# Kernel tuning notes

Hardware: AMD Instinct MI355X
Metric: run time of the kernel (lower is better)

The kernel has to match this reference:

```python
import jax, jax.numpy as jnp
import numpy as np

NEG_INF = -1e10
SLOPE = 0.01  # LeakyReLU default negative slope

def _lrelu(x):
    return jnp.where(x >= 0, x, SLOPE * x)

def setup_inputs() -> dict:
    key = jax.random.key(0)
    ks = jax.random.split(key, 12)
    B, L, D = 64, 512, 512
    s = 1.0 / np.sqrt(D)
    s2 = 1.0 / np.sqrt(2 * D)
    return {
        "r1": jax.random.normal(ks[0], (B, L, D), jnp.float32),
        "r2": jax.random.normal(ks[1], (B, L, D), jnp.float32),
        "mask1": jax.random.randint(ks[2], (B, L, 1), 0, 2, jnp.int32),
        "mask2": jax.random.randint(ks[3], (B, L, 1), 0, 2, jnp.int32),
        # mlp params (shared for r1 and r2, as in the torch module)
        "W1": jax.random.uniform(ks[4], (D, D), jnp.float32, -s, s),
        "b1": jnp.zeros((D,), jnp.float32),
        "W2": jax.random.uniform(ks[5], (D, D), jnp.float32, -s, s),
        "b2": jnp.zeros((D,), jnp.float32),
        # compare params
        "Wc1": jax.random.uniform(ks[6], (2 * D, D), jnp.float32, -s2, s2),
        "bc1": jnp.zeros((D,), jnp.float32),
        "Wc2": jax.random.uniform(ks[7], (D, D), jnp.float32, -s, s),
        "bc2": jnp.zeros((D,), jnp.float32),
    }

def reference(r1, r2, mask1, mask2, W1, b1, W2, b2, Wc1, bc1, Wc2, bc2):
    # dropout is inference-mode identity
    def mlp(x):
        return _lrelu(_lrelu(x @ W1 + b1) @ W2 + b2)

    def compare(x):
        return _lrelu(_lrelu(x @ Wc1 + bc1) @ Wc2 + bc2)

    m1 = mask1.astype(jnp.float32)  # [B,L1,1]
    m2 = mask2.astype(jnp.float32)  # [B,L2,1]
    r1m = mlp(r1) * m1
    r2m = mlp(r2) * m2

    # pairwise mask: >0 iff both tokens valid (magnitude from the D-dim matmul is irrelevant)
    mpos = m1 * jnp.swapaxes(m2, 1, 2)            # [B,L1,L2] in {0,1}
    mask_inf = jnp.where(mpos > 0, 0.0, NEG_INF)  # additive mask

    o = jnp.einsum('bik,bjk->bij', r1m, r2m) + mask_inf  # [B,L1,L2]
    o1 = jax.nn.softmax(o, axis=2) * mpos
    o2 = jax.nn.softmax(o, axis=1) * mpos

    r1_c = jnp.einsum('bij,bjd->bid', o1, r2m)  # [B,L1,D]
    r2_c = jnp.einsum('bij,bid->bjd', o2, r1m)  # [B,L2,D]

    r1_cmp = compare(jnp.concatenate([r1m, r1_c], axis=-1)) * m1
    r2_cmp = compare(jnp.concatenate([r2m, r2_c], axis=-1)) * m2
    return (r1_cmp, r2_cmp)
```

## Files before the change

### kernel.cpp

```cpp
#include <hip/hip_runtime.h>

#define LRELU_SLOPE 0.01f
#define NEG_BIG -1e10f

typedef unsigned short ushort_t;
typedef __bf16 bf16x8 __attribute__((ext_vector_type(8)));
typedef float f32x4 __attribute__((ext_vector_type(4)));

static __device__ __forceinline__ float lrelu_f(float x) {
    return x >= 0.0f ? x : LRELU_SLOPE * x;
}

static __device__ __forceinline__ ushort_t f2bf(float f) {
    unsigned int u = __float_as_uint(f);
    u += 0x7fffu + ((u >> 16) & 1u);
    return (ushort_t)(u >> 16);
}

static __device__ __forceinline__ void gld_lds16(const ushort_t* g, ushort_t* l) {
    __builtin_amdgcn_global_load_lds((const __attribute__((address_space(1))) void*)g,
                                     (__attribute__((address_space(3))) void*)l,
                                     16, 0, 0);
}

template<bool BIAS, bool LRELU, bool RM, bool PM, bool BF16OUT, bool TWOUT>
__global__ __launch_bounds__(512, 4)
void gemm_nt(const ushort_t* __restrict__ A0, const ushort_t* __restrict__ A1,
             int Ksplit, int lda0, int lda1,
             const ushort_t* __restrict__ B, int ldb,
             const float* __restrict__ bias,
             const int* __restrict__ rm1, const int* __restrict__ rm2,
             void* __restrict__ C, int ldc,
             ushort_t* __restrict__ CT, int Mhalf,
             int M, int N, int K,
             long sA, long sB, long sC)
{
    __shared__ ushort_t As[256 * 64];
    __shared__ ushort_t Bs[128 * 64];

    const unsigned nbx = gridDim.x, nby = gridDim.y;
    unsigned lin = blockIdx.x + nbx * (blockIdx.y + nby * blockIdx.z);
    const unsigned nwg = nbx * nby * gridDim.z;
    if ((nwg & 7u) == 0u)
        lin = (lin & 7u) * (nwg >> 3) + (lin >> 3);
    const unsigned bxs = lin % nbx;
    const unsigned t1  = lin / nbx;
    const unsigned bys = t1 % nby;
    const unsigned bzs = t1 / nby;

    const int bz   = (int)bzs;
    const int tid  = threadIdx.x;
    const int w    = tid >> 6;
    const int lane = tid & 63;
    const int wm   = w >> 1;
    const int wn   = w & 1;
    const int row0 = (int)bys * 256;
    const int col0 = (int)bxs * 128;

    const ushort_t* Ab0 = A0 + (long)bz * sA;
    const ushort_t* Ab1 = A1 + (long)bz * sA;
    const ushort_t* Bb  = B  + (long)bz * sB;

    const int srA = w * 32 + (lane >> 3);
    const int srB = w * 16 + (lane >> 3);
    const int so  = (((lane & 7) ^ ((lane >> 3) & 7)) * 8);

    const int lr = lane & 15, q = lane >> 4;
    const int cx0 = ((q ^ (lr & 7)) * 8);
    const int cx1 = (((q + 4) ^ (lr & 7)) * 8);
    const int aRow = (wm * 64 + lr) * 64;
    const int bRow = (wn * 64 + lr) * 64;

    f32x4 acc[4][4] = {};

    auto stage = [&](int T) {
        const int k0g = T << 6;
        const ushort_t* Ap; int kk0, ldaP;
        if (k0g < Ksplit) { Ap = Ab0; kk0 = k0g;          ldaP = lda0; }
        else              { Ap = Ab1; kk0 = k0g - Ksplit; ldaP = lda1; }
        #pragma unroll
        for (int u = 0; u < 4; ++u)
            gld_lds16(Ap + (size_t)(row0 + srA + u * 8) * ldaP + kk0 + so,
                      As + (w * 32 + u * 8) * 64);
        #pragma unroll
        for (int u = 0; u < 2; ++u)
            gld_lds16(Bb + (size_t)(col0 + srB + u * 8) * ldb + k0g + so,
                      Bs + (w * 16 + u * 8) * 64);
    };

    const int NT = K >> 6;

    for (int T = 0; T < NT; ++T) {
        __builtin_amdgcn_s_barrier();
        asm volatile("" ::: "memory");
        stage(T);
        asm volatile("s_waitcnt vmcnt(0)" ::: "memory");
        __builtin_amdgcn_s_barrier();
        asm volatile("" ::: "memory");

        #pragma unroll
        for (int kk = 0; kk < 2; ++kk) {
            const int cx = kk ? cx1 : cx0;
            bf16x8 af[4], bf[4];
            #pragma unroll
            for (int ii = 0; ii < 4; ++ii)
                af[ii] = *reinterpret_cast<const bf16x8*>(&As[aRow + (ii * 16) * 64 + cx]);
            #pragma unroll
            for (int jj = 0; jj < 4; ++jj)
                bf[jj] = *reinterpret_cast<const bf16x8*>(&Bs[bRow + (jj * 16) * 64 + cx]);
            asm volatile("s_waitcnt lgkmcnt(0)" ::: "memory");
            __builtin_amdgcn_sched_barrier(0);
            __builtin_amdgcn_s_setprio(1);
            #pragma unroll
            for (int ii = 0; ii < 4; ++ii)
                #pragma unroll
                for (int jj = 0; jj < 4; ++jj)
                    acc[ii][jj] = __builtin_amdgcn_mfma_f32_16x16x32_bf16(
                        af[ii], bf[jj], acc[ii][jj], 0, 0, 0);
            __builtin_amdgcn_s_setprio(0);
        }
    }

    float biasv[4];
    int mj[4];
    #pragma unroll
    for (int j = 0; j < 4; ++j) {
        const int c = col0 + wn * 64 + j * 16 + lr;
        if (BIAS) biasv[j] = bias[c];
        if (PM)   mj[j] = rm2[(long)bz * N + c];
    }
    float* Cf = (float*)C + (long)bz * sC;
    ushort_t* Ch = (ushort_t*)C + (long)bz * sC;

    #pragma unroll
    for (int i = 0; i < 4; ++i) {
        const int rg0 = row0 + wm * 64 + i * 16 + q * 4;
        int mi4[4];
        if (RM || PM) {
            #pragma unroll
            for (int r = 0; r < 4; ++r) {
                const int row = rg0 + r;
                if (PM)      mi4[r] = rm1[(long)bz * M + row];
                else         mi4[r] = (row < Mhalf) ? rm1[row] : rm2[row - Mhalf];
            }
        }
        #pragma unroll
        for (int j = 0; j < 4; ++j) {
            const int c = col0 + wn * 64 + j * 16 + lr;
            ushort_t tp[4];
            #pragma unroll
            for (int r = 0; r < 4; ++r) {
                const int row = rg0 + r;
                float v = acc[i][j][r];
                if (BIAS) v += biasv[j];
                if (LRELU) v = lrelu_f(v);
                if (RM) v *= (float)mi4[r];
                if (PM) { if (!(mi4[r] && mj[j])) v += NEG_BIG; }
                const size_t a = (size_t)row * ldc + c;
                if (BF16OUT) Ch[a] = f2bf(v); else Cf[a] = v;
                if (TWOUT) tp[r] = f2bf(v);
            }
            if (TWOUT) {
                const size_t ta = ((size_t)(((rg0 >> 9) + 64) & 127)) * 262144
                                + (size_t)c * 512 + (rg0 & 511);
                *reinterpret_cast<uint2*>(CT + ta) = *reinterpret_cast<uint2*>(tp);
            }
        }
    }
}

__global__ __launch_bounds__(256)
void cvt2_f32_bf16(const float* __restrict__ a, const float* __restrict__ b,
                   ushort_t* __restrict__ oa, ushort_t* __restrict__ ob)
{
    const float* in = blockIdx.y ? b : a;
    ushort_t* out = blockIdx.y ? ob : oa;
    const long i = ((long)blockIdx.x * 256 + threadIdx.x) * 4;
    const float4 v = *reinterpret_cast<const float4*>(in + i);
    ushort_t o[4] = { f2bf(v.x), f2bf(v.y), f2bf(v.z), f2bf(v.w) };
    *reinterpret_cast<uint2*>(out + i) = *reinterpret_cast<uint2*>(o);
}

__global__ __launch_bounds__(256)
void transpose_cvt4(const float* __restrict__ W1, const float* __restrict__ W2,
                    const float* __restrict__ Wc1, const float* __restrict__ Wc2,
                    ushort_t* __restrict__ W1t, ushort_t* __restrict__ W2t,
                    ushort_t* __restrict__ Wc1t, ushort_t* __restrict__ Wc2t)
{
    __shared__ float t[32][33];
    const int z = blockIdx.z;
    const float* in = (z == 0) ? W1 : (z == 1) ? W2 : (z == 2) ? Wc1 : Wc2;
    ushort_t* out   = (z == 0) ? W1t : (z == 1) ? W2t : (z == 2) ? Wc1t : Wc2t;
    const int R = (z == 2) ? 1024 : 512;
    const int C = 512;
    const int c0 = blockIdx.x * 32, r0 = blockIdx.y * 32;
    if (r0 >= R) return;
    const int tx = threadIdx.x & 31, ty = threadIdx.x >> 5;
    #pragma unroll
    for (int p = 0; p < 4; ++p)
        t[ty + p * 8][tx] = in[(size_t)(r0 + ty + p * 8) * C + c0 + tx];
    __syncthreads();
    #pragma unroll
    for (int p = 0; p < 4; ++p)
        out[(size_t)(c0 + ty + p * 8) * R + r0 + tx] = f2bf(t[tx][ty + p * 8]);
}

__global__ __launch_bounds__(256)
void row_stats(const float* __restrict__ o, float* __restrict__ rmax,
               float* __restrict__ rsinv, int L)
{
    const int row  = blockIdx.x * 4 + (threadIdx.x >> 6);
    const int lane = threadIdx.x & 63;
    const float* p = o + (long)row * L;
    float m = -3.0e38f;
    for (int j = lane; j < L; j += 64) m = fmaxf(m, p[j]);
    #pragma unroll
    for (int off = 32; off > 0; off >>= 1) m = fmaxf(m, __shfl_xor(m, off));
    float s = 0.0f;
    for (int j = lane; j < L; j += 64) s += __expf(p[j] - m);
    #pragma unroll
    for (int off = 32; off > 0; off >>= 1) s += __shfl_xor(s, off);
    if (lane == 0) { rmax[row] = m; rsinv[row] = 1.0f / s; }
}

__global__ __launch_bounds__(256)
void col_part(const float* __restrict__ o, float* __restrict__ pm,
              float* __restrict__ ps, int L)
{
    const int b  = blockIdx.z;
    const int rc = blockIdx.y;
    const int j  = blockIdx.x * 256 + threadIdx.x;
    const float* p = o + (long)b * L * L + (long)rc * 64 * L + j;
    float m = -3.0e38f, s = 0.0f;
    #pragma unroll 4
    for (int i = 0; i < 64; ++i) {
        const float x = p[(long)i * L];
        const float mn = fmaxf(m, x);
        s = s * __expf(m - mn) + __expf(x - mn);
        m = mn;
    }
    const long idx = ((long)b * 8 + rc) * L + j;
    pm[idx] = m;
    ps[idx] = s;
}

__global__ __launch_bounds__(256)
void col_combine(const float* __restrict__ pm, const float* __restrict__ ps,
                 float* __restrict__ cmax, float* __restrict__ csinv, int L)
{
    const int b = blockIdx.y;
    const int j = blockIdx.x * 256 + threadIdx.x;
    float mk[8], sk[8];
    #pragma unroll
    for (int k = 0; k < 8; ++k) {
        mk[k] = pm[((long)b * 8 + k) * L + j];
        sk[k] = ps[((long)b * 8 + k) * L + j];
    }
    float m = -3.0e38f;
    #pragma unroll
    for (int k = 0; k < 8; ++k) m = fmaxf(m, mk[k]);
    float s = 0.0f;
    #pragma unroll
    for (int k = 0; k < 8; ++k) s += sk[k] * __expf(mk[k] - m);
    cmax[b * L + j]  = m;
    csinv[b * L + j] = 1.0f / s;
}

__global__ __launch_bounds__(256)
void softmax_apply(const float* __restrict__ o,
                   ushort_t* __restrict__ o1, ushort_t* __restrict__ o2T,
                   const float* __restrict__ rmax, const float* __restrict__ rsinv,
                   const float* __restrict__ cmax, const float* __restrict__ csinv,
                   const int* __restrict__ m1, const int* __restrict__ m2)
{
    __shared__ ushort_t t[32][33];
    const int b = blockIdx.z;
    const long bo = (long)b * 512 * 512;
    const int j0 = blockIdx.x * 32, i0 = blockIdx.y * 32;
    const int tx = threadIdx.x & 31, ty = threadIdx.x >> 5;
    const int col = b * 512 + j0 + tx;
    const int mjv = m2[col];
    const float cm = cmax[col], cs = csinv[col];
    #pragma unroll
    for (int p = 0; p < 4; ++p) {
        const int i = i0 + ty + p * 8;
        const int row = b * 512 + i;
        const float x = o[bo + (long)i * 512 + j0 + tx];
        const float mp = (m1[row] != 0 && mjv != 0) ? 1.0f : 0.0f;
        o1[bo + (long)i * 512 + j0 + tx] = f2bf(__expf(x - rmax[row]) * rsinv[row] * mp);
        t[ty + p * 8][tx] = f2bf(__expf(x - cm) * cs * mp);
    }
    __syncthreads();
    #pragma unroll
    for (int p = 0; p < 4; ++p)
        o2T[bo + (long)(j0 + ty + p * 8) * 512 + i0 + tx] = t[tx][ty + p * 8];
}

extern "C" void kernel_launch(void* const* d_in, const int* in_sizes, int n_in,
                              void* d_out, int out_size, void* d_ws, size_t ws_size,
                              hipStream_t stream)
{
    const float* r1  = (const float*)d_in[0];
    const float* r2  = (const float*)d_in[1];
    const int*   m1  = (const int*)d_in[2];
    const int*   m2  = (const int*)d_in[3];
    const float* W1  = (const float*)d_in[4];
    const float* b1v = (const float*)d_in[5];
    const float* W2  = (const float*)d_in[6];
    const float* b2v = (const float*)d_in[7];
    const float* Wc1 = (const float*)d_in[8];
    const float* bc1 = (const float*)d_in[9];
    const float* Wc2 = (const float*)d_in[10];
    const float* bc2 = (const float*)d_in[11];
    float* out = (float*)d_out;

    constexpr int  Bn = 64, L = 512, D = 512;
    constexpr long CE = (long)Bn * L * D;
    constexpr long S  = (long)L * L;
    constexpr int  NR = Bn * L;

    ushort_t* O    = (ushort_t*)d_out;
    ushort_t* r1b  = O;
    ushort_t* r2b  = O + CE;
    ushort_t* TT   = O;
    ushort_t* o1b  = O + 2 * CE;
    ushort_t* o2Tb = O + 3 * CE;

    char* wsb = (char*)d_ws;
    ushort_t* hb   = (ushort_t*)wsb;
    float*    obuf = (float*)wsb;
    ushort_t* r1c  = (ushort_t*)wsb;
    ushort_t* hc   = (ushort_t*)(wsb + 4 * CE);
    ushort_t* r1mb = (ushort_t*)(wsb + 8 * CE);
    ushort_t* r2mb = (ushort_t*)(wsb + 10 * CE);
    ushort_t* W1t  = (ushort_t*)(wsb + 12 * CE);
    ushort_t* W2t  = W1t + 512 * 512;
    ushort_t* Wc1t = W2t + 512 * 512;
    ushort_t* Wc2t = Wc1t + 512 * 1024;
    float* rmaxv = (float*)(Wc2t + 512 * 512);
    float* rsinv = rmaxv + NR;
    float* cmaxv = rsinv + NR;
    float* csinv = cmaxv + NR;
    float* pmbuf = csinv + NR;
    float* psbuf = pmbuf + 8 * L * Bn;

    const dim3 blk(256);
    const dim3 blkG(512);
    const dim3 gD2(D / 128, 2 * NR / 256, 1);
    const dim3 gB(L / 128, L / 256, Bn);
    const dim3 gB2(L / 128, L / 256, 2 * Bn);

    cvt2_f32_bf16<<<dim3(CE / 1024, 2), blk, 0, stream>>>(r1, r2, r1b, r2b);
    transpose_cvt4<<<dim3(16, 32, 4), blk, 0, stream>>>(
        W1, W2, Wc1, Wc2, W1t, W2t, Wc1t, Wc2t);

    gemm_nt<true,true,false,false,true,false><<<gD2, blkG, 0, stream>>>(
        r1b, r1b, D, D, D, W1t, D, b1v, nullptr, nullptr, hb, D,
        nullptr, 0, 2 * NR, D, D, 0, 0, 0);
    gemm_nt<true,true,true,false,true,true><<<gD2, blkG, 0, stream>>>(
        hb, hb, D, D, D, W2t, D, b2v, m1, m2, r1mb, D,
        TT, NR, 2 * NR, D, D, 0, 0, 0);
    gemm_nt<false,false,false,true,false,false><<<gB, blkG, 0, stream>>>(
        r1mb, r1mb, D, D, D, r2mb, D, nullptr, m1, m2, obuf, L,
        nullptr, 0, L, L, D, S, S, S);
    row_stats<<<dim3(NR / 4), blk, 0, stream>>>(obuf, rmaxv, rsinv, L);
    col_part<<<dim3(L / 256, 8, Bn), blk, 0, stream>>>(obuf, pmbuf, psbuf, L);
    col_combine<<<dim3(L / 256, Bn), blk, 0, stream>>>(pmbuf, psbuf, cmaxv, csinv, L);
    softmax_apply<<<dim3(16, 16, Bn), blk, 0, stream>>>(
        obuf, o1b, o2Tb, rmaxv, rsinv, cmaxv, csinv, m1, m2);
    gemm_nt<false,false,false,false,true,false><<<gB2, blkG, 0, stream>>>(
        o1b, o1b, L, L, L, TT, L, nullptr, nullptr, nullptr, r1c, D,
        nullptr, 0, L, D, L, S, S, S);
    gemm_nt<true,true,false,false,true,false><<<gD2, blkG, 0, stream>>>(
        r1mb, r1c, D, D, D, Wc1t, 2 * D, bc1, nullptr, nullptr, hc, D,
        nullptr, 0, 2 * NR, D, 2 * D, 0, 0, 0);
    gemm_nt<true,true,true,false,false,false><<<gD2, blkG, 0, stream>>>(
        hc, hc, D, D, D, Wc2t, D, bc2, m1, m2, out, D,
        nullptr, NR, 2 * NR, D, D, 0, 0, 0);
}
```

Baseline: 599.6 us.

## Restructure GEMM to stage full-K B panel in LDS and stream A from global

Measured after the change: 1.010 ms. 68.4% more time.

```diff
diff --git a/kernel.cpp b/kernel.cpp
--- a/kernel.cpp
+++ b/kernel.cpp
@@ -35,8 +35,7 @@
              int M, int N, int K,
              long sA, long sB, long sC)
 {
-    __shared__ ushort_t As[256 * 64];
-    __shared__ ushort_t Bs[128 * 64];
+    __shared__ ushort_t Bs[64 * 512];
 
     const unsigned nbx = gridDim.x, nby = gridDim.y;
     unsigned lin = blockIdx.x + nbx * (blockIdx.y + nby * blockIdx.z);
@@ -52,72 +51,53 @@
     const int tid  = threadIdx.x;
     const int w    = tid >> 6;
     const int lane = tid & 63;
-    const int wm   = w >> 1;
-    const int wn   = w & 1;
-    const int row0 = (int)bys * 256;
-    const int col0 = (int)bxs * 128;
-
-    const ushort_t* Ab0 = A0 + (long)bz * sA;
-    const ushort_t* Ab1 = A1 + (long)bz * sA;
-    const ushort_t* Bb  = B  + (long)bz * sB;
-
-    const int srA = w * 32 + (lane >> 3);
-    const int srB = w * 16 + (lane >> 3);
-    const int so  = (((lane & 7) ^ ((lane >> 3) & 7)) * 8);
+    const int row0 = (int)bys * 512;
+    const int col0 = (int)bxs * 64;
 
     const int lr = lane & 15, q = lane >> 4;
-    const int cx0 = ((q ^ (lr & 7)) * 8);
-    const int cx1 = (((q + 4) ^ (lr & 7)) * 8);
-    const int aRow = (wm * 64 + lr) * 64;
-    const int bRow = (wn * 64 + lr) * 64;
+    const int wrow = row0 + w * 64;
+
+    const ushort_t* Bb = B + (long)bz * sB;
 
     f32x4 acc[4][4] = {};
 
-    auto stage = [&](int T) {
-        const int k0g = T << 6;
-        const ushort_t* Ap; int kk0, ldaP;
-        if (k0g < Ksplit) { Ap = Ab0; kk0 = k0g;          ldaP = lda0; }
-        else              { Ap = Ab1; kk0 = k0g - Ksplit; ldaP = lda1; }
+    const int nch = K >> 9;
+    for (int ch = 0; ch < nch; ++ch) {
+        const ushort_t* Ap = (ch == 0) ? A0 + (long)bz * sA : A1 + (long)bz * sA;
+        const int lda = (ch == 0) ? lda0 : lda1;
+        const int kb  = ch << 9;
+
+        if (ch) {
+            __builtin_amdgcn_s_barrier();
+            asm volatile("" ::: "memory");
+        }
         #pragma unroll
-        for (int u = 0; u < 4; ++u)
-            gld_lds16(Ap + (size_t)(row0 + srA + u * 8) * ldaP + kk0 + so,
-                      As + (w * 32 + u * 8) * 64);
-        #pragma unroll
-        for (int u = 0; u < 2; ++u)
-            gld_lds16(Bb + (size_t)(col0 + srB + u * 8) * ldb + k0g + so,
-                      Bs + (w * 16 + u * 8) * 64);
-    };
-
-    const int NT = K >> 6;
-
-    for (int T = 0; T < NT; ++T) {
-        __builtin_amdgcn_s_barrier();
-        asm volatile("" ::: "memory");
-        stage(T);
+        for (int r = 0; r < 8; ++r) {
+            const int brow = w * 8 + r;
+            gld_lds16(Bb + (size_t)(col0 + brow) * ldb + kb + ((lane ^ (r & 7)) * 8),
+                      &Bs[brow * 512]);
+        }
         asm volatile("s_waitcnt vmcnt(0)" ::: "memory");
         __builtin_amdgcn_s_barrier();
         asm volatile("" ::: "memory");
 
         #pragma unroll
-        for (int kk = 0; kk < 2; ++kk) {
-            const int cx = kk ? cx1 : cx0;
+        for (int ks = 0; ks < 16; ++ks) {
             bf16x8 af[4], bf[4];
             #pragma unroll
             for (int ii = 0; ii < 4; ++ii)
-                af[ii] = *reinterpret_cast<const bf16x8*>(&As[aRow + (ii * 16) * 64 + cx]);
+                af[ii] = *reinterpret_cast<const bf16x8*>(
+                    &Ap[(size_t)(wrow + ii * 16 + lr) * lda + ks * 32 + q * 8]);
             #pragma unroll
             for (int jj = 0; jj < 4; ++jj)
-                bf[jj] = *reinterpret_cast<const bf16x8*>(&Bs[bRow + (jj * 16) * 64 + cx]);
-            asm volatile("s_waitcnt lgkmcnt(0)" ::: "memory");
-            __builtin_amdgcn_sched_barrier(0);
-            __builtin_amdgcn_s_setprio(1);
+                bf[jj] = *reinterpret_cast<const bf16x8*>(
+                    &Bs[(jj * 16 + lr) * 512 + (((ks * 4 + q) ^ (lr & 7)) * 8)]);
             #pragma unroll
             for (int ii = 0; ii < 4; ++ii)
                 #pragma unroll
                 for (int jj = 0; jj < 4; ++jj)
                     acc[ii][jj] = __builtin_amdgcn_mfma_f32_16x16x32_bf16(
                         af[ii], bf[jj], acc[ii][jj], 0, 0, 0);
-            __builtin_amdgcn_s_setprio(0);
         }
     }
 
@@ -125,7 +105,7 @@
     int mj[4];
     #pragma unroll
     for (int j = 0; j < 4; ++j) {
-        const int c = col0 + wn * 64 + j * 16 + lr;
+        const int c = col0 + j * 16 + lr;
         if (BIAS) biasv[j] = bias[c];
         if (PM)   mj[j] = rm2[(long)bz * N + c];
     }
@@ -134,7 +114,7 @@
 
     #pragma unroll
     for (int i = 0; i < 4; ++i) {
-        const int rg0 = row0 + wm * 64 + i * 16 + q * 4;
+        const int rg0 = wrow + i * 16 + q * 4;
         int mi4[4];
         if (RM || PM) {
             #pragma unroll
@@ -146,7 +126,7 @@
         }
         #pragma unroll
         for (int j = 0; j < 4; ++j) {
-            const int c = col0 + wn * 64 + j * 16 + lr;
+            const int c = col0 + j * 16 + lr;
             ushort_t tp[4];
             #pragma unroll
             for (int r = 0; r < 4; ++r) {
@@ -346,9 +326,9 @@
 
     const dim3 blk(256);
     const dim3 blkG(512);
-    const dim3 gD2(D / 128, 2 * NR / 256, 1);
-    const dim3 gB(L / 128, L / 256, Bn);
-    const dim3 gB2(L / 128, L / 256, 2 * Bn);
+    const dim3 gD2(D / 64, 2 * NR / 512, 1);
+    const dim3 gB(L / 64, L / 512, Bn);
+    const dim3 gB2(L / 64, L / 512, 2 * Bn);
 
     cvt2_f32_bf16<<<dim3(CE / 1024, 2), blk, 0, stream>>>(r1, r2, r1b, r2b);
     transpose_cvt4<<<dim3(16, 32, 4), blk, 0, stream>>>(
```
